# Kernel optimization log

Hardware: AMD Instinct MI355X
Metric: run time of the kernel (lower is better)

The kernel has to match this reference:

```python
import jax, jax.numpy as jnp
import numpy as np

B, C, D, DE, NH = 4, 4, 96, 96, 3
NS, HIN, TOTAL_Z, PZ = 12, 128, 64, 32
WZ = WH = WW = 4
N_WIN_TOK = WZ * WH * WW  # 64 tokens per 3D window


def _rel_index():
    # standard Swin-3D relative position index, (N, N) into a (7*7*7, NH) table
    c = np.stack(np.meshgrid(np.arange(WZ), np.arange(WH), np.arange(WW), indexing='ij')).reshape(3, -1)
    r = (c[:, :, None] - c[:, None, :]).transpose(1, 2, 0)
    r += np.array([WZ - 1, WH - 1, WW - 1])
    r[:, :, 0] *= (2 * WH - 1) * (2 * WW - 1)
    r[:, :, 1] *= (2 * WW - 1)
    return jnp.asarray(r.sum(-1))

REL_IDX = _rel_index()


def layernorm(x, g, b, eps=1e-5):
    m = x.mean(-1, keepdims=True)
    v = x.var(-1, keepdims=True)
    return (x - m) * jax.lax.rsqrt(v + eps) * g + b


def groupnorm(x, g, b, groups=8, eps=1e-5):
    Bb, Cc, Z, H, W = x.shape
    xr = x.reshape(Bb, groups, Cc // groups, Z, H, W)
    m = xr.mean((2, 3, 4, 5), keepdims=True)
    v = xr.var((2, 3, 4, 5), keepdims=True)
    xr = (xr - m) * jax.lax.rsqrt(v + eps)
    return xr.reshape(Bb, Cc, Z, H, W) * g[None, :, None, None, None] + b[None, :, None, None, None]


def conv3d(x, w, b):
    y = jax.lax.conv_general_dilated(x, w, (1, 1, 1), 'SAME', dimension_numbers=('NCDHW', 'OIDHW', 'NCDHW'))
    return y + b[None, :, None, None, None]


def z_interp(x, pos, out_z):
    """Linear interp along z. x:(B,C,S,H,W), pos:(S,) sorted float positions.
    Matches the torch loop: clamp below first / above last, weight=0.5 on ties."""
    S = x.shape[2]
    zq = jnp.arange(out_z, dtype=jnp.float32)
    right = jnp.searchsorted(pos, zq, side='left')  # first i with pos[i] >= z
    left = jnp.clip(right - 1, 0, S - 1)
    rc = jnp.clip(right, 0, S - 1)
    lp, rp = pos[left], pos[rc]
    d = rp - lp
    w = jnp.where(d > 0, (zq - lp) / jnp.where(d > 0, d, 1.0), 0.5)
    w = w[None, None, :, None, None]
    return (1.0 - w) * x[:, :, left] + w * x[:, :, rc]


def reference(sparse_obs, encoder_feat, pe_w, pe_b, pe_g, pe_beta, enc_w, enc_b, ln_g, ln_b,
              qkv_w, qkv_b, attn_w, attn_b, rpb, ref_w1, ref_b1, gn1_g, gn1_b,
              ref_w2, ref_b2, gn2_g, gn2_b, rec_w, rec_b, sparse_indices):
    Bb, Cc, Sz, H, W = sparse_obs.shape
    pos = sparse_indices.astype(jnp.float32)
    # --- skip connection: z-interp baseline at full resolution ---
    baseline = z_interp(sparse_obs, pos, TOTAL_Z)  # (B,C,64,128,128)
    # --- sparse patch embed: conv (1,4,4) stride (1,4,4) + LN ---
    xr = sparse_obs.reshape(Bb, Cc, Sz, H // 4, 4, W // 4, 4)
    f = jnp.einsum('bczhpwq,dcpq->bdzhw', xr, pe_w) + pe_b[None, :, None, None, None]
    f = layernorm(f.transpose(0, 2, 3, 4, 1), pe_g, pe_beta).transpose(0, 4, 1, 2, 3)
    # position-aware z interpolation into patch space (patch_size_z = 2)
    f = z_interp(f, pos / 2.0, PZ)  # (B,D,32,32,32)
    # --- encoder 1x1x1 projection + fuse ---
    enc = jnp.einsum('bczhw,dc->bdzhw', encoder_feat, enc_w) + enc_b[None, :, None, None, None]
    f = f + enc
    # --- 3D window attention with relative position bias (pre-norm, residual) ---
    nz = PZ // WZ
    x = f.transpose(0, 2, 3, 4, 1)  # (B,Z,H,W,D)
    xw = x.reshape(Bb, nz, WZ, nz, WH, nz, WW, D).transpose(0, 1, 3, 5, 2, 4, 6, 7).reshape(-1, N_WIN_TOK, D)
    sc = xw
    xn = layernorm(xw, ln_g, ln_b)
    dh = D // NH
    qkv = (xn @ qkv_w.T + qkv_b).reshape(-1, N_WIN_TOK, 3, NH, dh).transpose(2, 0, 3, 1, 4)
    q, k, v = qkv[0], qkv[1], qkv[2]  # (nWin*B, NH, N, dh)
    att = jnp.einsum('whnd,whmd->whnm', q * (dh ** -0.5), k)
    att = att + rpb[REL_IDX].transpose(2, 0, 1)[None]  # (.., NH, N, N)
    att = jax.nn.softmax(att, axis=-1)
    o = jnp.einsum('whnm,whmd->whnd', att, v).transpose(0, 2, 1, 3).reshape(-1, N_WIN_TOK, D)
    xw = sc + (o @ attn_w.T + attn_b)
    x = xw.reshape(Bb, nz, nz, nz, WZ, WH, WW, D).transpose(0, 1, 4, 2, 5, 3, 6, 7).reshape(Bb, PZ, PZ, PZ, D)
    f = x.transpose(0, 4, 1, 2, 3)
    f = jax.nn.gelu(groupnorm(conv3d(f, ref_w1, ref_b1), gn1_g, gn1_b), approximate=False)
    f = jax.nn.gelu(groupnorm(conv3d(f, ref_w2, ref_b2), gn2_g, gn2_b), approximate=False)
    # --- patch recovery: ConvTranspose3d kernel=stride=(2,4,4) as einsum+reshape ---
    delta = jnp.einsum('bizhw,iodef->bozdhewf', f, rec_w).reshape(Bb, Cc, PZ * 2, PZ * 4, PZ * 4)
    delta = delta + rec_b[None, :, None, None, None]
    return baseline + delta


def setup_inputs():
    key = jax.random.key(0)
    ks = jax.random.split(key, 16)
    n = lambda i, shape: jax.random.normal(ks[i], shape, dtype=jnp.float32) * 0.02
    return {
        'sparse_obs': jax.random.normal(ks[0], (B, C, NS, HIN, HIN), dtype=jnp.float32),
        'encoder_feat': jax.random.normal(ks[1], (B, DE, PZ, PZ, PZ), dtype=jnp.float32),
        'pe_w': n(2, (D, C, 4, 4)), 'pe_b': jnp.zeros((D,)), 'pe_g': jnp.ones((D,)), 'pe_beta': jnp.zeros((D,)),
        'enc_w': n(3, (D, DE)), 'enc_b': jnp.zeros((D,)),
        'ln_g': jnp.ones((D,)), 'ln_b': jnp.zeros((D,)),
        'qkv_w': n(4, (3 * D, D)), 'qkv_b': jnp.zeros((3 * D,)),
        'attn_w': n(5, (D, D)), 'attn_b': jnp.zeros((D,)),
        'rpb': n(6, ((2 * WZ - 1) * (2 * WH - 1) * (2 * WW - 1), NH)),
        'ref_w1': n(7, (D, D, 3, 3, 3)), 'ref_b1': jnp.zeros((D,)), 'gn1_g': jnp.ones((D,)), 'gn1_b': jnp.zeros((D,)),
        'ref_w2': n(8, (D, D, 3, 3, 3)), 'ref_b2': jnp.zeros((D,)), 'gn2_g': jnp.ones((D,)), 'gn2_b': jnp.zeros((D,)),
        'rec_w': n(9, (D, C, 2, 4, 4)), 'rec_b': jnp.zeros((C,)),
        'sparse_indices': jnp.asarray(np.round(np.linspace(0, 63, 12)).astype(np.int64)),
    }
```

## Files before the change

kernel.cpp:

```cpp
#include <hip/hip_runtime.h>
#include <math.h>

typedef __attribute__((ext_vector_type(8))) short short8v;
typedef __attribute__((ext_vector_type(4))) float float4v;

__device__ inline unsigned short f2bf(float f) {
  unsigned u = __float_as_uint(f);
  return (unsigned short)((u + 0x7fff + ((u >> 16) & 1)) >> 16);
}
__device__ inline unsigned pk2(float a, float b) {
  return (unsigned)f2bf(a) | ((unsigned)f2bf(b) << 16);
}
__device__ inline float bfl(unsigned u) { return __uint_as_float(u << 16); }
__device__ inline float bfh(unsigned u) { return __uint_as_float(u & 0xffff0000u); }
__device__ inline float bfs(short s) { return __uint_as_float(((unsigned)(unsigned short)s) << 16); }

__global__ __launch_bounds__(96) void k_tables(const int* __restrict__ sidx, int* __restrict__ T) {
  __shared__ float pos[12];
  int t = threadIdx.x;
  if (t < 12) pos[t] = (float)sidx[t];
  __syncthreads();
  if (t < 64) {
    float zq = (float)t;
    int r = 0;
    while (r < 12 && pos[r] < zq) r++;
    int l = r - 1; if (l < 0) l = 0; if (l > 11) l = 11;
    int rc = r; if (rc > 11) rc = 11;
    float lp = pos[l], rp = pos[rc], d = rp - lp;
    float w = d > 0.f ? (zq - lp) / d : 0.5f;
    T[t] = l; T[64 + t] = rc; ((float*)T)[128 + t] = w;
  } else {
    int zq = t - 64;
    float zqf = (float)zq;
    int r = 0;
    while (r < 12 && pos[r] * 0.5f < zqf) r++;
    int l = r - 1; if (l < 0) l = 0; if (l > 11) l = 11;
    int rc = r; if (rc > 11) rc = 11;
    float lp = pos[l] * 0.5f, rp = pos[rc] * 0.5f, d = rp - lp;
    float w = d > 0.f ? (zqf - lp) / d : 0.5f;
    T[192 + zq] = l; T[224 + zq] = rc; ((float*)T)[256 + zq] = w;
  }
}

__global__ __launch_bounds__(256) void k_wcv(const float* __restrict__ w, short* __restrict__ Wt) {
  int id = blockIdx.x * 256 + threadIdx.x;
  if (id >= 248832) return;
  float v = w[id];
  int o = id / 2592; int rem = id % 2592; int i = rem / 27; int tap = rem % 27;
  Wt[(tap * 96 + o) * 96 + i] = (short)f2bf(v);
}

__global__ __launch_bounds__(256) void k_cvt(const float* __restrict__ src, short* __restrict__ dst, int n) {
  int id = blockIdx.x * 256 + threadIdx.x;
  if (id < n) dst[id] = (short)f2bf(src[id]);
}

__global__ __launch_bounds__(256) void k_wrt(const float* __restrict__ src, short* __restrict__ dst) {
  int id = blockIdx.x * 256 + threadIdx.x;
  if (id >= 12288) return;
  int i = id >> 7, j = id & 127;
  dst[j * 96 + i] = (short)f2bf(src[id]);
}

__global__ __launch_bounds__(256) void k_bias(const float* __restrict__ rpb, float* __restrict__ Bt) {
  int id = blockIdx.x * 256 + threadIdx.x;
  if (id >= 12288) return;
  int head = id >> 12, rem = id & 4095, n = rem >> 6, m = rem & 63;
  int dz = (n >> 4) - (m >> 4), dh = ((n >> 2) & 3) - ((m >> 2) & 3), dw = (n & 3) - (m & 3);
  Bt[id] = rpb[((dz + 3) * 49 + (dh + 3) * 7 + (dw + 3)) * 3 + head];
}

__global__ __launch_bounds__(256) void k_pe(const float* __restrict__ sp, const short* __restrict__ Wpe,
    const float* __restrict__ pb, const float* __restrict__ pg, const float* __restrict__ pbeta,
    float* __restrict__ f1) {
  int x = blockIdx.x;
  int b = x / 384, z = (x / 32) % 12, h = x % 32;
  __shared__ short sB[32][72];
  __shared__ float sF[32][97];
  __shared__ float sM[32], sR[32];
  int tid = threadIdx.x;
  for (int id = tid; id < 2048; id += 256) {
    int c = id >> 9, p = (id >> 7) & 3, col = id & 127;
    float v = sp[(((b * 4 + c) * 12 + z) * 128 + h * 4 + p) * 128 + col];
    sB[col >> 2][c * 16 + p * 4 + (col & 3)] = (short)f2bf(v);
  }
  __syncthreads();
  int w = tid >> 6, l = tid & 63, lo = l & 15, ig = l >> 4;
  int nt = w & 1, mbase = (w >> 1) * 3;
  short8v bfrag[2];
  #pragma unroll
  for (int kc = 0; kc < 2; kc++)
    bfrag[kc] = *(const short8v*)&sB[nt * 16 + lo][kc * 32 + ig * 8];
  #pragma unroll
  for (int mi = 0; mi < 3; mi++) {
    int m = mbase + mi;
    float4v acc = (float4v){0.f, 0.f, 0.f, 0.f};
    #pragma unroll
    for (int kc = 0; kc < 2; kc++) {
      short8v a = *(const short8v*)(Wpe + (size_t)(m * 16 + lo) * 64 + kc * 32 + ig * 8);
      acc = __builtin_amdgcn_mfma_f32_16x16x32_bf16(a, bfrag[kc], acc, 0, 0, 0);
    }
    int wcoord = nt * 16 + lo;
    #pragma unroll
    for (int r = 0; r < 4; r++) {
      int d = m * 16 + ig * 4 + r;
      sF[wcoord][d] = acc[r] + pb[d];
    }
  }
  __syncthreads();
  if (tid < 32) {
    int wv = tid;
    float s = 0.f, ss = 0.f;
    for (int d = 0; d < 96; d++) { float v = sF[wv][d]; s += v; ss += v * v; }
    float m = s * (1.f / 96.f);
    float var = ss * (1.f / 96.f) - m * m;
    sM[wv] = m; sR[wv] = rsqrtf(var + 1e-5f);
  }
  __syncthreads();
  for (int id = tid; id < 3072; id += 256) {
    int d = id >> 5, wv = id & 31;
    float v = (sF[wv][d] - sM[wv]) * sR[wv] * pg[d] + pbeta[d];
    f1[(((b * 96 + d) * 12 + z) * 32 + h) * 32 + wv] = v;
  }
}

__global__ __launch_bounds__(256) void k_ie(const float* __restrict__ f1, const float* __restrict__ ef,
    const short* __restrict__ Wenc, const float* __restrict__ eb, const int* __restrict__ T,
    unsigned* __restrict__ Xg) {
  int x = blockIdx.x;
  int b = x >> 9, chunk = x & 511;
  int v0 = chunk * 64;
  int z = v0 >> 10, rp = v0 & 1023;
  int zl = T[192 + z], zr = T[224 + z];
  float wt = ((const float*)T)[256 + z];
  __shared__ short sEb[64][104];
  int tid = threadIdx.x;
  for (int id = tid; id < 6144; id += 256) {
    int c = id >> 6, vs = id & 63;
    sEb[vs][c] = (short)f2bf(ef[(size_t)(b * 96 + c) * 32768 + v0 + vs]);
  }
  __syncthreads();
  int w = tid >> 6, l = tid & 63, lo = l & 15, ig = l >> 4;
  int vcol = w * 16 + lo;
  short8v bfrag[3];
  #pragma unroll
  for (int kc = 0; kc < 3; kc++)
    bfrag[kc] = *(const short8v*)&sEb[vcol][kc * 32 + ig * 8];
  float4v acc[6];
  #pragma unroll
  for (int m = 0; m < 6; m++) {
    acc[m] = (float4v){0.f, 0.f, 0.f, 0.f};
    #pragma unroll
    for (int kc = 0; kc < 3; kc++) {
      short8v a = *(const short8v*)(Wenc + (size_t)(m * 16 + lo) * 96 + kc * 32 + ig * 8);
      acc[m] = __builtin_amdgcn_mfma_f32_16x16x32_bf16(a, bfrag[kc], acc[m], 0, 0, 0);
    }
  }
  int zb = z >> 2, tz = z & 3;
  int h0 = (chunk & 15) * 2;
  int h = h0 + (vcol >> 5), wc = vcol & 31;
  int win = ((b * 8 + zb) * 8 + (h >> 2)) * 8 + (wc >> 2);
  int t = tz * 16 + (h & 3) * 4 + (wc & 3);
  size_t xbase = (size_t)(win * 64 + t) * 48;
  float wl = 1.f - wt;
  #pragma unroll
  for (int m = 0; m < 6; m++) {
    #pragma unroll
    for (int rr = 0; rr < 2; rr++) {
      int d0 = m * 16 + ig * 4 + rr * 2;
      const float* p1a = f1 + ((size_t)(b * 96 + d0) * 12 + zl) * 1024 + rp + vcol;
      const float* p2a = f1 + ((size_t)(b * 96 + d0) * 12 + zr) * 1024 + rp + vcol;
      const float* p1b = f1 + ((size_t)(b * 96 + d0 + 1) * 12 + zl) * 1024 + rp + vcol;
      const float* p2b = f1 + ((size_t)(b * 96 + d0 + 1) * 12 + zr) * 1024 + rp + vcol;
      float va = acc[m][rr * 2] + eb[d0] + wl * p1a[0] + wt * p2a[0];
      float vb = acc[m][rr * 2 + 1] + eb[d0 + 1] + wl * p1b[0] + wt * p2b[0];
      Xg[xbase + m * 8 + ig * 2 + rr] = pk2(va, vb);
    }
  }
}

__global__ __launch_bounds__(256) void k_fatt(const unsigned* __restrict__ Xg,
    const short* __restrict__ Wq, const float* __restrict__ qb,
    const float* __restrict__ lg, const float* __restrict__ lb,
    const short* __restrict__ Wa, const float* __restrict__ ab,
    const float* __restrict__ Bt, short* __restrict__ Xt) {
  int win = blockIdx.x;
  __shared__ short sA[64][104];
  __shared__ short sN[64][104];
  __shared__ short sK[192][40];
  __shared__ short sVt[96][88];
  __shared__ short sQP[4][16][104];
  __shared__ float sMn[64], sRs[64];
  int tid = threadIdx.x;
  int w = tid >> 6, l = tid & 63, lo = l & 15, ig = l >> 4;
  const float scale = 0.17677669529663687f;

  for (int id = tid; id < 3072; id += 256) {
    int row = id / 48, c2 = id % 48;
    *(unsigned*)&sA[row][c2 * 2] = Xg[(size_t)(win * 64 + row) * 48 + c2];
  }
  __syncthreads();
  {
    int token = tid >> 2, jl = tid & 3;
    float s = 0.f, ss = 0.f;
    #pragma unroll
    for (int i = 0; i < 12; i++) {
      unsigned u = *(unsigned*)&sA[token][jl * 24 + i * 2];
      float v0 = bfl(u), v1 = bfh(u);
      s += v0 + v1; ss += v0 * v0 + v1 * v1;
    }
    s += __shfl_xor(s, 1); ss += __shfl_xor(ss, 1);
    s += __shfl_xor(s, 2); ss += __shfl_xor(ss, 2);
    if (jl == 0) {
      float m = s * (1.f / 96.f);
      sMn[token] = m;
      sRs[token] = rsqrtf(ss * (1.f / 96.f) - m * m + 1e-5f);
    }
  }
  __syncthreads();
  for (int id = tid; id < 3072; id += 256) {
    int row = id / 48, c2 = id % 48;
    unsigned u = *(unsigned*)&sA[row][c2 * 2];
    float m = sMn[row], r = sRs[row];
    float v0 = (bfl(u) - m) * r * lg[2 * c2] + lb[2 * c2];
    float v1 = (bfh(u) - m) * r * lg[2 * c2 + 1] + lb[2 * c2 + 1];
    *(unsigned*)&sN[row][c2 * 2] = pk2(v0, v1);
  }
  __syncthreads();
  {
    short8v a[3];
    #pragma unroll
    for (int kc = 0; kc < 3; kc++)
      a[kc] = *(const short8v*)&sN[w * 16 + lo][kc * 32 + ig * 8];
    for (int nt = 0; nt < 18; nt++) {
      float4v acc = (float4v){0.f, 0.f, 0.f, 0.f};
      #pragma unroll
      for (int kc = 0; kc < 3; kc++) {
        short8v bfr = *(const short8v*)(Wq + (size_t)(nt * 16 + lo) * 96 + kc * 32 + ig * 8);
        acc = __builtin_amdgcn_mfma_f32_16x16x32_bf16(a[kc], bfr, acc, 0, 0, 0);
      }
      int out = nt * 16 + lo;
      float bias = qb[out];
      if (nt < 6) {
        int head = out >> 5, c = out & 31;
        #pragma unroll
        for (int r = 0; r < 4; r++)
          sQP[w][ig * 4 + r][head * 32 + c] = (short)f2bf((acc[r] + bias) * scale);
      } else if (nt < 12) {
        int o2 = out - 96, head = o2 >> 5, c = o2 & 31;
        #pragma unroll
        for (int r = 0; r < 4; r++)
          sK[head * 64 + w * 16 + ig * 4 + r][c] = (short)f2bf(acc[r] + bias);
      } else {
        int o2 = out - 192;
        #pragma unroll
        for (int r = 0; r < 4; r++)
          sVt[o2][w * 16 + ig * 4 + r] = (short)f2bf(acc[r] + bias);
      }
    }
  }
  __syncthreads();
  short8v qf[3];
  #pragma unroll
  for (int h = 0; h < 3; h++)
    qf[h] = *(const short8v*)&sQP[w][lo][h * 32 + ig * 8];
  for (int h = 0; h < 3; h++) {
    short8v kf[4];
    #pragma unroll
    for (int nt = 0; nt < 4; nt++)
      kf[nt] = *(const short8v*)&sK[h * 64 + nt * 16 + lo][ig * 8];
    float4v s[4];
    #pragma unroll
    for (int nt = 0; nt < 4; nt++)
      s[nt] = __builtin_amdgcn_mfma_f32_16x16x32_bf16(qf[h], kf[nt], (float4v){0.f, 0.f, 0.f, 0.f}, 0, 0, 0);
    const float* bt = Bt + h * 4096;
    #pragma unroll
    for (int r = 0; r < 4; r++) {
      int tok = w * 16 + ig * 4 + r;
      float v[4];
      float mx = -1e30f;
      #pragma unroll
      for (int nt = 0; nt < 4; nt++) {
        v[nt] = s[nt][r] + bt[tok * 64 + nt * 16 + lo];
        mx = fmaxf(mx, v[nt]);
      }
      mx = fmaxf(mx, __shfl_xor(mx, 1));
      mx = fmaxf(mx, __shfl_xor(mx, 2));
      mx = fmaxf(mx, __shfl_xor(mx, 4));
      mx = fmaxf(mx, __shfl_xor(mx, 8));
      float sm = 0.f;
      #pragma unroll
      for (int nt = 0; nt < 4; nt++) { v[nt] = __expf(v[nt] - mx); sm += v[nt]; }
      sm += __shfl_xor(sm, 1);
      sm += __shfl_xor(sm, 2);
      sm += __shfl_xor(sm, 4);
      sm += __shfl_xor(sm, 8);
      float inv = 1.f / sm;
      #pragma unroll
      for (int nt = 0; nt < 4; nt++)
        sQP[w][ig * 4 + r][nt * 16 + lo] = (short)f2bf(v[nt] * inv);
    }
    short8v pa[2];
    #pragma unroll
    for (int kc = 0; kc < 2; kc++)
      pa[kc] = *(const short8v*)&sQP[w][lo][kc * 32 + ig * 8];
    #pragma unroll
    for (int ct = 0; ct < 2; ct++) {
      short8v vb0 = *(const short8v*)&sVt[h * 32 + ct * 16 + lo][ig * 8];
      short8v vb1 = *(const short8v*)&sVt[h * 32 + ct * 16 + lo][32 + ig * 8];
      float4v o = __builtin_amdgcn_mfma_f32_16x16x32_bf16(pa[0], vb0, (float4v){0.f, 0.f, 0.f, 0.f}, 0, 0, 0);
      o = __builtin_amdgcn_mfma_f32_16x16x32_bf16(pa[1], vb1, o, 0, 0, 0);
      #pragma unroll
      for (int r = 0; r < 4; r++)
        sA[w * 16 + ig * 4 + r][h * 32 + ct * 16 + lo] = (short)f2bf(o[r]);
    }
  }
  {
    short8v a[3];
    #pragma unroll
    for (int kc = 0; kc < 3; kc++)
      a[kc] = *(const short8v*)&sA[w * 16 + lo][kc * 32 + ig * 8];
    #pragma unroll
    for (int nt = 0; nt < 6; nt++) {
      float4v acc = (float4v){0.f, 0.f, 0.f, 0.f};
      #pragma unroll
      for (int kc = 0; kc < 3; kc++) {
        short8v bfr = *(const short8v*)(Wa + (size_t)(nt * 16 + lo) * 96 + kc * 32 + ig * 8);
        acc = __builtin_amdgcn_mfma_f32_16x16x32_bf16(a[kc], bfr, acc, 0, 0, 0);
      }
      int out = nt * 16 + lo;
      float bias = ab[out];
      #pragma unroll
      for (int r = 0; r < 4; r++) {
        int tok = w * 16 + ig * 4 + r;
        unsigned u = Xg[(size_t)(win * 64 + tok) * 48 + (out >> 1)];
        float res = (out & 1) ? bfh(u) : bfl(u);
        sN[tok][out] = (short)f2bf(acc[r] + bias + res);
      }
    }
  }
  __syncthreads();
  int b = win >> 9, zb = (win >> 6) & 7, hb = (win >> 3) & 7, wb = win & 7;
  for (int id = tid; id < 3072; id += 256) {
    int cc = id >> 10, rem = id & 1023, t = rem >> 4, ilp = rem & 15;
    unsigned pk = *(unsigned*)&sN[t][cc * 32 + ilp * 2];
    int tz = t >> 4, th = (t >> 2) & 3, tw = t & 3;
    size_t vox = (size_t)(zb * 4 + tz) * 1024 + (hb * 4 + th) * 32 + wb * 4 + tw;
    ((unsigned*)Xt)[((size_t)(b * 3 + cc) * 32768 + vox) * 16 + ilp] = pk;
  }
}

__global__ __launch_bounds__(256) void k_convM(const short* __restrict__ Xt,
    const short* __restrict__ Wt, const float* __restrict__ cb, short* __restrict__ y16,
    float* __restrict__ stats) {
  int x = blockIdx.x;
  int b = x >> 7, zp = (x >> 3) & 15, hq = x & 7;
  int tid = threadIdx.x;
  int wvi = tid >> 6, l = tid & 63;
  int lo = l & 15, ig = l >> 4;
  int hp = wvi & 1, mh = wvi >> 1;
  __shared__ short Xl[816 * 32];
  __shared__ float sG[16];
  if (tid < 16) sG[tid] = 0.f;
  float4v acc[3][2][2][2];
  #pragma unroll
  for (int mi = 0; mi < 3; mi++)
    #pragma unroll
    for (int zo = 0; zo < 2; zo++)
      #pragma unroll
      for (int hr = 0; hr < 2; hr++)
        #pragma unroll
        for (int n = 0; n < 2; n++) acc[mi][zo][hr][n] = (float4v){0.f, 0.f, 0.f, 0.f};

  for (int c = 0; c < 3; c++) {
    __syncthreads();
    for (int r = 0; r < 13; r++) {
      int id = tid + 256 * r;
      if (id < 3264) {
        int seg = id & 3, q = id >> 2;
        int zz = q / 204, rem = q - zz * 204;
        int hh = rem / 34, ww = rem - hh * 34;
        int gz = zp * 2 + zz - 1, gh = hq * 4 + hh - 1, gw = ww - 1;
        int4 val = {0, 0, 0, 0};
        if (gz >= 0 && gz < 32 && gh >= 0 && gh < 32 && gw >= 0 && gw < 32)
          val = *(const int4*)(Xt + ((size_t)((b * 3 + c) * 32768 + (gz << 10) + (gh << 5) + gw) * 32 + seg * 8));
        int slot = seg ^ ((q >> 1) & 3);
        *(int4*)(&Xl[q * 32 + slot * 8]) = val;
      }
    }
    __syncthreads();
    for (int dh = 0; dh < 3; dh++) {
      for (int dwv = 0; dwv < 3; dwv++) {
        short8v bfr[4][2][2];
        #pragma unroll
        for (int zr = 0; zr < 4; zr++)
          #pragma unroll
          for (int hr = 0; hr < 2; hr++)
            #pragma unroll
            for (int n = 0; n < 2; n++) {
              int vox = (zr * 6 + hp * 2 + hr + dh) * 34 + n * 16 + lo + dwv;
              bfr[zr][hr][n] = *(const short8v*)&Xl[vox * 32 + ((ig ^ ((vox >> 1) & 3)) * 8)];
            }
        #pragma unroll
        for (int dz = 0; dz < 3; dz++) {
          int tap = dz * 9 + dh * 3 + dwv;
          #pragma unroll
          for (int mi = 0; mi < 3; mi++) {
            short8v wf = *(const short8v*)(Wt +
                ((size_t)(tap * 96 + (mh * 3 + mi) * 16 + lo)) * 96 + c * 32 + ig * 8);
            #pragma unroll
            for (int zo = 0; zo < 2; zo++)
              #pragma unroll
              for (int hr = 0; hr < 2; hr++)
                #pragma unroll
                for (int n = 0; n < 2; n++)
                  acc[mi][zo][hr][n] = __builtin_amdgcn_mfma_f32_16x16x32_bf16(wf, bfr[zo + dz][hr][n], acc[mi][zo][hr][n], 0, 0, 0);
          }
        }
      }
    }
  }
  #pragma unroll
  for (int mi = 0; mi < 3; mi++) {
    #pragma unroll
    for (int r = 0; r < 4; r++) {
      int o = (mh * 3 + mi) * 16 + ig * 4 + r;
      float cbo = cb[o];
      float s = 0.f, ss = 0.f;
      #pragma unroll
      for (int zo = 0; zo < 2; zo++)
        #pragma unroll
        for (int hr = 0; hr < 2; hr++)
          #pragma unroll
          for (int n = 0; n < 2; n++) {
            float v = acc[mi][zo][hr][n][r] + cbo;
            int z = zp * 2 + zo;
            int h = hq * 4 + hp * 2 + hr;
            int vcol = n * 16 + lo;
            y16[((size_t)(b * 96 + o) << 15) + (z << 10) + (h << 5) + vcol] = (short)f2bf(v);
            s += v; ss += v * v;
          }
      s += __shfl_xor(s, 1); ss += __shfl_xor(ss, 1);
      s += __shfl_xor(s, 2); ss += __shfl_xor(ss, 2);
      s += __shfl_xor(s, 4); ss += __shfl_xor(ss, 4);
      s += __shfl_xor(s, 8); ss += __shfl_xor(ss, 8);
      if (lo == 0) {
        int gl = o / 12;
        atomicAdd(&sG[gl * 2], s);
        atomicAdd(&sG[gl * 2 + 1], ss);
      }
    }
  }
  __syncthreads();
  if (tid < 16) atomicAdd(&stats[b * 16 + tid], sG[tid]);
}

__global__ __launch_bounds__(256) void k_gn(const short* __restrict__ y16, const float* __restrict__ stats,
    const float* __restrict__ gg, const float* __restrict__ gb, short* __restrict__ xt) {
  int x = blockIdx.x;
  int b = x / 1536, r = x % 1536, c = r / 512, vt = r % 512;
  int v0 = vt * 64;
  __shared__ float sT[64][33];
  int tid = threadIdx.x;
  const float invN = 1.f / 393216.f;
  {
    int ol = tid >> 3, vq = tid & 7;
    int o = c * 32 + ol, g = b * 8 + o / 12;
    float m = stats[2 * g] * invN;
    float var = stats[2 * g + 1] * invN - m * m;
    float rs = rsqrtf(var + 1e-5f) * gg[o];
    float bb = gb[o];
    short8v yv = *(const short8v*)&y16[((size_t)(b * 96 + o) << 15) + v0 + vq * 8];
    #pragma unroll
    for (int j = 0; j < 8; j++) {
      float val = (bfs(yv[j]) - m) * rs + bb;
      sT[vq * 8 + j][ol] = 0.5f * val * (1.f + erff(val * 0.70710678118654752f));
    }
  }
  __syncthreads();
  for (int id = tid; id < 1024; id += 256) {
    int v = id >> 4, p = id & 15;
    ((unsigned*)xt)[((size_t)(b * 3 + c) * 32768 + v0 + v) * 16 + p] = pk2(sT[v][2 * p], sT[v][2 * p + 1]);
  }
}

__global__ __launch_bounds__(256) void k_final(const short* __restrict__ f5b, const float* __restrict__ sp,
    const short* __restrict__ Wrec, const float* __restrict__ rb, const int* __restrict__ T,
    float* __restrict__ out) {
  int x = blockIdx.x;
  int b = x >> 10, chunk = x & 1023;
  int z = chunk >> 5, h = chunk & 31;
  int v0 = chunk * 32;
  int tid = threadIdx.x;
  int w = tid >> 6, l = tid & 63, lo = l & 15, ig = l >> 4;
  short8v afrag[2][3];
  #pragma unroll
  for (int mt = 0; mt < 2; mt++)
    #pragma unroll
    for (int kc = 0; kc < 3; kc++)
      afrag[mt][kc] = *(const short8v*)(f5b +
          ((size_t)(b * 3 + kc) * 32768 + v0 + mt * 16 + lo) * 32 + ig * 8);
  float4v acc[2][2];
  #pragma unroll
  for (int nt2 = 0; nt2 < 2; nt2++) {
    int jt = w * 2 + nt2;
    #pragma unroll
    for (int mt = 0; mt < 2; mt++) acc[mt][nt2] = (float4v){0.f, 0.f, 0.f, 0.f};
    #pragma unroll
    for (int kc = 0; kc < 3; kc++) {
      short8v bfr = *(const short8v*)(Wrec + (size_t)(jt * 16 + lo) * 96 + kc * 32 + ig * 8);
      #pragma unroll
      for (int mt = 0; mt < 2; mt++)
        acc[mt][nt2] = __builtin_amdgcn_mfma_f32_16x16x32_bf16(afrag[mt][kc], bfr, acc[mt][nt2], 0, 0, 0);
    }
  }
  const float* w64 = (const float*)(T + 128);
  #pragma unroll
  for (int mt = 0; mt < 2; mt++)
    #pragma unroll
    for (int nt2 = 0; nt2 < 2; nt2++) {
      int jt = w * 2 + nt2;
      #pragma unroll
      for (int r = 0; r < 4; r++) {
        int wv = mt * 16 + ig * 4 + r;
        int j = jt * 16 + lo;
        int o = j >> 5, dd = (j >> 4) & 1, e = (j >> 2) & 3, ff = j & 3;
        int Z = 2 * z + dd, H = 4 * h + e, W = 4 * wv + ff;
        int zl = T[Z], zr = T[64 + Z];
        float bw = w64[Z];
        const float* spb = sp + (size_t)(b * 4 + o) * 196608;
        float bval = (1.f - bw) * spb[(size_t)zl * 16384 + H * 128 + W]
                   + bw * spb[(size_t)zr * 16384 + H * 128 + W];
        out[((size_t)(b * 4 + o) * 64 + Z) * 16384 + H * 128 + W] = bval + acc[mt][nt2][r] + rb[o];
      }
    }
}

extern "C" void kernel_launch(void* const* d_in, const int* in_sizes, int n_in,
                              void* d_out, int out_size, void* d_ws, size_t ws_size,
                              hipStream_t stream) {
  const float* sp    = (const float*)d_in[0];
  const float* ef    = (const float*)d_in[1];
  const float* pe_w  = (const float*)d_in[2];
  const float* pe_b  = (const float*)d_in[3];
  const float* pe_g  = (const float*)d_in[4];
  const float* pe_be = (const float*)d_in[5];
  const float* enc_w = (const float*)d_in[6];
  const float* enc_b = (const float*)d_in[7];
  const float* ln_g  = (const float*)d_in[8];
  const float* ln_b  = (const float*)d_in[9];
  const float* qkv_w = (const float*)d_in[10];
  const float* qkv_b = (const float*)d_in[11];
  const float* at_w  = (const float*)d_in[12];
  const float* at_b  = (const float*)d_in[13];
  const float* rpb   = (const float*)d_in[14];
  const float* w1    = (const float*)d_in[15];
  const float* b1    = (const float*)d_in[16];
  const float* g1g   = (const float*)d_in[17];
  const float* g1b   = (const float*)d_in[18];
  const float* w2    = (const float*)d_in[19];
  const float* b2    = (const float*)d_in[20];
  const float* g2g   = (const float*)d_in[21];
  const float* g2b   = (const float*)d_in[22];
  const float* recw  = (const float*)d_in[23];
  const float* recb  = (const float*)d_in[24];
  const int*   sidx  = (const int*)d_in[25];
  float* out = (float*)d_out;

  char* ws = (char*)d_ws;
  unsigned* Xg = (unsigned*)ws;
  float* f1    = (float*)(ws + 25165824);
  short* XtA   = (short*)(ws + 25165824);
  short* Y16   = (short*)(ws + 50331648);
  int*   T     = (int*)(ws + 100663296);
  float* stats = (float*)(ws + 100665344);
  short* Wrec  = (short*)(ws + 100666368);

  char* dob = (char*)d_out;
  short* Wenc = (short*)(dob + 25165824);
  short* Wpe  = (short*)(dob + 25184256);
  short* Wqkv = (short*)(dob + 65937408);
  short* Waw  = (short*)(dob + 65992704);
  float* Bt   = (float*)(dob + 66011136);
  short* Wt1  = (short*)(dob + 66060288);
  short* Wt2  = (short*)(dob + 66557952);

  k_tables<<<1, 96, 0, stream>>>(sidx, T);
  k_wcv<<<972, 256, 0, stream>>>(w1, Wt1);
  k_wcv<<<972, 256, 0, stream>>>(w2, Wt2);
  k_cvt<<<108, 256, 0, stream>>>(qkv_w, Wqkv, 27648);
  k_cvt<<<36, 256, 0, stream>>>(at_w, Waw, 9216);
  k_cvt<<<36, 256, 0, stream>>>(enc_w, Wenc, 9216);
  k_cvt<<<24, 256, 0, stream>>>(pe_w, Wpe, 6144);
  k_wrt<<<48, 256, 0, stream>>>(recw, Wrec);
  k_bias<<<48, 256, 0, stream>>>(rpb, Bt);

  k_pe<<<1536, 256, 0, stream>>>(sp, Wpe, pe_b, pe_g, pe_be, f1);
  k_ie<<<2048, 256, 0, stream>>>(f1, ef, Wenc, enc_b, T, Xg);
  k_fatt<<<2048, 256, 0, stream>>>(Xg, Wqkv, qkv_b, ln_g, ln_b, Waw, at_b, Bt, XtA);

  hipMemsetAsync(stats, 0, 64 * sizeof(float), stream);
  k_convM<<<512, 256, 0, stream>>>(XtA, Wt1, b1, Y16, stats);
  k_gn<<<6144, 256, 0, stream>>>(Y16, stats, g1g, g1b, XtA);

  hipMemsetAsync(stats, 0, 64 * sizeof(float), stream);
  k_convM<<<512, 256, 0, stream>>>(XtA, Wt2, b2, Y16, stats);
  k_gn<<<6144, 256, 0, stream>>>(Y16, stats, g2g, g2b, XtA);

  k_final<<<4096, 256, 0, stream>>>(XtA, sp, Wrec, recb, T, out);
}
```

Measured before the change: 359.9 us.

## Merge prep kernels, fold layernorm into QKV load, split conv work across more blocks

Nine small weight-conversion and table kernels become a single k_prep launch to cut launch overhead. In the attention kernel the separate layernorm pass and its sN buffer are removed: normalization is applied while loading the MFMA A fragments. The K buffer is unpadded and uses an XOR swizzle, which shrinks LDS. The 3D conv now splits output channels into halves across twice as many blocks, with each wave handling one z slice, so it needs fewer accumulators. This may raise occupancy, at the cost of loading each input halo tile twice.

```diff
diff --git a/kernel.cpp b/kernel.cpp
--- a/kernel.cpp
+++ b/kernel.cpp
@@ -15,59 +15,80 @@
 __device__ inline float bfh(unsigned u) { return __uint_as_float(u & 0xffff0000u); }
 __device__ inline float bfs(short s) { return __uint_as_float(((unsigned)(unsigned short)s) << 16); }
 
-__global__ __launch_bounds__(96) void k_tables(const int* __restrict__ sidx, int* __restrict__ T) {
-  __shared__ float pos[12];
-  int t = threadIdx.x;
-  if (t < 12) pos[t] = (float)sidx[t];
-  __syncthreads();
-  if (t < 64) {
-    float zq = (float)t;
-    int r = 0;
-    while (r < 12 && pos[r] < zq) r++;
-    int l = r - 1; if (l < 0) l = 0; if (l > 11) l = 11;
-    int rc = r; if (rc > 11) rc = 11;
-    float lp = pos[l], rp = pos[rc], d = rp - lp;
-    float w = d > 0.f ? (zq - lp) / d : 0.5f;
-    T[t] = l; T[64 + t] = rc; ((float*)T)[128 + t] = w;
+__global__ __launch_bounds__(256) void k_prep(
+    const int* __restrict__ sidx, int* __restrict__ T,
+    const float* __restrict__ w1, short* __restrict__ Wt1,
+    const float* __restrict__ w2, short* __restrict__ Wt2,
+    const float* __restrict__ qkvw, short* __restrict__ Wqkv,
+    const float* __restrict__ atw, short* __restrict__ Waw,
+    const float* __restrict__ encw, short* __restrict__ Wenc,
+    const float* __restrict__ pew, short* __restrict__ Wpe,
+    const float* __restrict__ recw, short* __restrict__ Wrec,
+    const float* __restrict__ rpb, float* __restrict__ Bt) {
+  int bx = blockIdx.x;
+  int tid = threadIdx.x;
+  if (bx < 1944) {
+    const float* w = bx < 972 ? w1 : w2;
+    short* Wt = bx < 972 ? Wt1 : Wt2;
+    int id = (bx < 972 ? bx : bx - 972) * 256 + tid;
+    if (id < 248832) {
+      float v = w[id];
+      int o = id / 2592; int rem = id % 2592; int i = rem / 27; int tap = rem % 27;
+      Wt[(tap * 96 + o) * 96 + i] = (short)f2bf(v);
+    }
+  } else if (bx < 2052) {
+    int id = (bx - 1944) * 256 + tid;
+    if (id < 27648) Wqkv[id] = (short)f2bf(qkvw[id]);
+  } else if (bx < 2088) {
+    int id = (bx - 2052) * 256 + tid;
+    if (id < 9216) Waw[id] = (short)f2bf(atw[id]);
+  } else if (bx < 2124) {
+    int id = (bx - 2088) * 256 + tid;
+    if (id < 9216) Wenc[id] = (short)f2bf(encw[id]);
+  } else if (bx < 2148) {
+    int id = (bx - 2124) * 256 + tid;
+    if (id < 6144) Wpe[id] = (short)f2bf(pew[id]);
+  } else if (bx < 2196) {
+    int id = (bx - 2148) * 256 + tid;
+    if (id < 12288) {
+      int i = id >> 7, j = id & 127;
+      Wrec[j * 96 + i] = (short)f2bf(recw[id]);
+    }
+  } else if (bx < 2244) {
+    int id = (bx - 2196) * 256 + tid;
+    if (id < 12288) {
+      int head = id >> 12, rem = id & 4095, n = rem >> 6, m = rem & 63;
+      int dz = (n >> 4) - (m >> 4), dh = ((n >> 2) & 3) - ((m >> 2) & 3), dw = (n & 3) - (m & 3);
+      Bt[id] = rpb[((dz + 3) * 49 + (dh + 3) * 7 + (dw + 3)) * 3 + head];
+    }
   } else {
-    int zq = t - 64;
-    float zqf = (float)zq;
-    int r = 0;
-    while (r < 12 && pos[r] * 0.5f < zqf) r++;
-    int l = r - 1; if (l < 0) l = 0; if (l > 11) l = 11;
-    int rc = r; if (rc > 11) rc = 11;
-    float lp = pos[l] * 0.5f, rp = pos[rc] * 0.5f, d = rp - lp;
-    float w = d > 0.f ? (zqf - lp) / d : 0.5f;
-    T[192 + zq] = l; T[224 + zq] = rc; ((float*)T)[256 + zq] = w;
-  }
-}
-
-__global__ __launch_bounds__(256) void k_wcv(const float* __restrict__ w, short* __restrict__ Wt) {
-  int id = blockIdx.x * 256 + threadIdx.x;
-  if (id >= 248832) return;
-  float v = w[id];
-  int o = id / 2592; int rem = id % 2592; int i = rem / 27; int tap = rem % 27;
-  Wt[(tap * 96 + o) * 96 + i] = (short)f2bf(v);
-}
-
-__global__ __launch_bounds__(256) void k_cvt(const float* __restrict__ src, short* __restrict__ dst, int n) {
-  int id = blockIdx.x * 256 + threadIdx.x;
-  if (id < n) dst[id] = (short)f2bf(src[id]);
-}
-
-__global__ __launch_bounds__(256) void k_wrt(const float* __restrict__ src, short* __restrict__ dst) {
-  int id = blockIdx.x * 256 + threadIdx.x;
-  if (id >= 12288) return;
-  int i = id >> 7, j = id & 127;
-  dst[j * 96 + i] = (short)f2bf(src[id]);
-}
-
-__global__ __launch_bounds__(256) void k_bias(const float* __restrict__ rpb, float* __restrict__ Bt) {
-  int id = blockIdx.x * 256 + threadIdx.x;
-  if (id >= 12288) return;
-  int head = id >> 12, rem = id & 4095, n = rem >> 6, m = rem & 63;
-  int dz = (n >> 4) - (m >> 4), dh = ((n >> 2) & 3) - ((m >> 2) & 3), dw = (n & 3) - (m & 3);
-  Bt[id] = rpb[((dz + 3) * 49 + (dh + 3) * 7 + (dw + 3)) * 3 + head];
+    __shared__ float pos[12];
+    int t = tid;
+    if (t < 12) pos[t] = (float)sidx[t];
+    __syncthreads();
+    if (t < 64) {
+      float zq = (float)t;
+      int r = 0;
+      while (r < 12 && pos[r] < zq) r++;
+      int lft = r - 1; if (lft < 0) lft = 0; if (lft > 11) lft = 11;
+      int rc = r; if (rc > 11) rc = 11;
+      float lp = pos[lft], rp = pos[rc], d = rp - lp;
+      float w = d > 0.f ? (zq - lp) / d : 0.5f;
+      T[t] = lft; T[64 + t] = rc; ((float*)T)[128 + t] = w;
+    } else if (t < 128) {
+      int zq = t - 64;
+      float zqf = (float)zq;
+      if (zq < 32) {
+        int r = 0;
+        while (r < 12 && pos[r] * 0.5f < zqf) r++;
+        int lft = r - 1; if (lft < 0) lft = 0; if (lft > 11) lft = 11;
+        int rc = r; if (rc > 11) rc = 11;
+        float lp = pos[lft] * 0.5f, rp = pos[rc] * 0.5f, d = rp - lp;
+        float w = d > 0.f ? (zqf - lp) / d : 0.5f;
+        T[192 + zq] = lft; T[224 + zq] = rc; ((float*)T)[256 + zq] = w;
+      }
+    }
+  }
 }
 
 __global__ __launch_bounds__(256) void k_pe(const float* __restrict__ sp, const short* __restrict__ Wpe,
@@ -186,10 +207,9 @@
     const float* __restrict__ Bt, short* __restrict__ Xt) {
   int win = blockIdx.x;
   __shared__ short sA[64][104];
-  __shared__ short sN[64][104];
-  __shared__ short sK[192][40];
-  __shared__ short sVt[96][88];
-  __shared__ short sQP[4][16][104];
+  __shared__ short sQP[4][16][96];
+  __shared__ short sK[192][32];
+  __shared__ short sVt[96][72];
   __shared__ float sMn[64], sRs[64];
   int tid = threadIdx.x;
   int w = tid >> 6, l = tid & 63, lo = l & 15, ig = l >> 4;
@@ -218,20 +238,22 @@
     }
   }
   __syncthreads();
-  for (int id = tid; id < 3072; id += 256) {
-    int row = id / 48, c2 = id % 48;
-    unsigned u = *(unsigned*)&sA[row][c2 * 2];
-    float m = sMn[row], r = sRs[row];
-    float v0 = (bfl(u) - m) * r * lg[2 * c2] + lb[2 * c2];
-    float v1 = (bfh(u) - m) * r * lg[2 * c2 + 1] + lb[2 * c2 + 1];
-    *(unsigned*)&sN[row][c2 * 2] = pk2(v0, v1);
-  }
-  __syncthreads();
   {
+    int tok = w * 16 + lo;
+    float m = sMn[tok], rr = sRs[tok];
     short8v a[3];
     #pragma unroll
-    for (int kc = 0; kc < 3; kc++)
-      a[kc] = *(const short8v*)&sN[w * 16 + lo][kc * 32 + ig * 8];
+    for (int kc = 0; kc < 3; kc++) {
+      short8v raw = *(const short8v*)&sA[tok][kc * 32 + ig * 8];
+      short8v t;
+      #pragma unroll
+      for (int jj = 0; jj < 8; jj++) {
+        int c = kc * 32 + ig * 8 + jj;
+        float v = (bfs(raw[jj]) - m) * rr * lg[c] + lb[c];
+        t[jj] = (short)f2bf(v);
+      }
+      a[kc] = t;
+    }
     for (int nt = 0; nt < 18; nt++) {
       float4v acc = (float4v){0.f, 0.f, 0.f, 0.f};
       #pragma unroll
@@ -249,8 +271,11 @@
       } else if (nt < 12) {
         int o2 = out - 96, head = o2 >> 5, c = o2 & 31;
         #pragma unroll
-        for (int r = 0; r < 4; r++)
-          sK[head * 64 + w * 16 + ig * 4 + r][c] = (short)f2bf(acc[r] + bias);
+        for (int r = 0; r < 4; r++) {
+          int row = head * 64 + w * 16 + ig * 4 + r;
+          ((short*)sK)[row * 32 + (((c >> 3) ^ ((row >> 1) & 3)) << 3) + (c & 7)] =
+              (short)f2bf(acc[r] + bias);
+        }
       } else {
         int o2 = out - 192;
         #pragma unroll
@@ -267,8 +292,10 @@
   for (int h = 0; h < 3; h++) {
     short8v kf[4];
     #pragma unroll
-    for (int nt = 0; nt < 4; nt++)
-      kf[nt] = *(const short8v*)&sK[h * 64 + nt * 16 + lo][ig * 8];
+    for (int nt = 0; nt < 4; nt++) {
+      int row = h * 64 + nt * 16 + lo;
+      kf[nt] = *(const short8v*)&((short*)sK)[row * 32 + ((ig ^ ((row >> 1) & 3)) << 3)];
+    }
     float4v s[4];
     #pragma unroll
     for (int nt = 0; nt < 4; nt++)
@@ -335,7 +362,7 @@
         int tok = w * 16 + ig * 4 + r;
         unsigned u = Xg[(size_t)(win * 64 + tok) * 48 + (out >> 1)];
         float res = (out & 1) ? bfh(u) : bfl(u);
-        sN[tok][out] = (short)f2bf(acc[r] + bias + res);
+        sA[tok][out] = (short)f2bf(acc[r] + bias + res);
       }
     }
   }
@@ -343,7 +370,7 @@
   int b = win >> 9, zb = (win >> 6) & 7, hb = (win >> 3) & 7, wb = win & 7;
   for (int id = tid; id < 3072; id += 256) {
     int cc = id >> 10, rem = id & 1023, t = rem >> 4, ilp = rem & 15;
-    unsigned pk = *(unsigned*)&sN[t][cc * 32 + ilp * 2];
+    unsigned pk = *(unsigned*)&sA[t][cc * 32 + ilp * 2];
     int tz = t >> 4, th = (t >> 2) & 3, tw = t & 3;
     size_t vox = (size_t)(zb * 4 + tz) * 1024 + (hb * 4 + th) * 32 + wb * 4 + tw;
     ((unsigned*)Xt)[((size_t)(b * 3 + cc) * 32768 + vox) * 16 + ilp] = pk;
@@ -354,23 +381,21 @@
     const short* __restrict__ Wt, const float* __restrict__ cb, short* __restrict__ y16,
     float* __restrict__ stats) {
   int x = blockIdx.x;
-  int b = x >> 7, zp = (x >> 3) & 15, hq = x & 7;
+  int oh = x & 1, hq = (x >> 1) & 7, zp = (x >> 4) & 15, b = x >> 8;
   int tid = threadIdx.x;
   int wvi = tid >> 6, l = tid & 63;
   int lo = l & 15, ig = l >> 4;
-  int hp = wvi & 1, mh = wvi >> 1;
+  int hp = wvi & 1, zo = wvi >> 1;
   __shared__ short Xl[816 * 32];
   __shared__ float sG[16];
   if (tid < 16) sG[tid] = 0.f;
-  float4v acc[3][2][2][2];
+  float4v acc[3][2][2];
   #pragma unroll
   for (int mi = 0; mi < 3; mi++)
     #pragma unroll
-    for (int zo = 0; zo < 2; zo++)
-      #pragma unroll
-      for (int hr = 0; hr < 2; hr++)
-        #pragma unroll
-        for (int n = 0; n < 2; n++) acc[mi][zo][hr][n] = (float4v){0.f, 0.f, 0.f, 0.f};
+    for (int hr = 0; hr < 2; hr++)
+      #pragma unroll
+      for (int n = 0; n < 2; n++) acc[mi][hr][n] = (float4v){0.f, 0.f, 0.f, 0.f};
 
   for (int c = 0; c < 3; c++) {
     __syncthreads();
@@ -391,15 +416,15 @@
     __syncthreads();
     for (int dh = 0; dh < 3; dh++) {
       for (int dwv = 0; dwv < 3; dwv++) {
-        short8v bfr[4][2][2];
+        short8v bfr[3][2][2];
         #pragma unroll
-        for (int zr = 0; zr < 4; zr++)
+        for (int dzr = 0; dzr < 3; dzr++)
           #pragma unroll
           for (int hr = 0; hr < 2; hr++)
             #pragma unroll
             for (int n = 0; n < 2; n++) {
-              int vox = (zr * 6 + hp * 2 + hr + dh) * 34 + n * 16 + lo + dwv;
-              bfr[zr][hr][n] = *(const short8v*)&Xl[vox * 32 + ((ig ^ ((vox >> 1) & 3)) * 8)];
+              int vox = ((zo + dzr) * 6 + hp * 2 + hr + dh) * 34 + n * 16 + lo + dwv;
+              bfr[dzr][hr][n] = *(const short8v*)&Xl[vox * 32 + ((ig ^ ((vox >> 1) & 3)) * 8)];
             }
         #pragma unroll
         for (int dz = 0; dz < 3; dz++) {
@@ -407,39 +432,35 @@
           #pragma unroll
           for (int mi = 0; mi < 3; mi++) {
             short8v wf = *(const short8v*)(Wt +
-                ((size_t)(tap * 96 + (mh * 3 + mi) * 16 + lo)) * 96 + c * 32 + ig * 8);
+                ((size_t)(tap * 96 + oh * 48 + mi * 16 + lo)) * 96 + c * 32 + ig * 8);
             #pragma unroll
-            for (int zo = 0; zo < 2; zo++)
+            for (int hr = 0; hr < 2; hr++)
               #pragma unroll
-              for (int hr = 0; hr < 2; hr++)
-                #pragma unroll
-                for (int n = 0; n < 2; n++)
-                  acc[mi][zo][hr][n] = __builtin_amdgcn_mfma_f32_16x16x32_bf16(wf, bfr[zo + dz][hr][n], acc[mi][zo][hr][n], 0, 0, 0);
+              for (int n = 0; n < 2; n++)
+                acc[mi][hr][n] = __builtin_amdgcn_mfma_f32_16x16x32_bf16(wf, bfr[dz][hr][n], acc[mi][hr][n], 0, 0, 0);
           }
         }
       }
     }
   }
+  int z = zp * 2 + zo;
   #pragma unroll
   for (int mi = 0; mi < 3; mi++) {
     #pragma unroll
     for (int r = 0; r < 4; r++) {
-      int o = (mh * 3 + mi) * 16 + ig * 4 + r;
+      int o = oh * 48 + mi * 16 + ig * 4 + r;
       float cbo = cb[o];
       float s = 0.f, ss = 0.f;
       #pragma unroll
-      for (int zo = 0; zo < 2; zo++)
+      for (int hr = 0; hr < 2; hr++)
         #pragma unroll
-        for (int hr = 0; hr < 2; hr++)
-          #pragma unroll
-          for (int n = 0; n < 2; n++) {
-            float v = acc[mi][zo][hr][n][r] + cbo;
-            int z = zp * 2 + zo;
-            int h = hq * 4 + hp * 2 + hr;
-            int vcol = n * 16 + lo;
-            y16[((size_t)(b * 96 + o) << 15) + (z << 10) + (h << 5) + vcol] = (short)f2bf(v);
-            s += v; ss += v * v;
-          }
+        for (int n = 0; n < 2; n++) {
+          float v = acc[mi][hr][n][r] + cbo;
+          int h = hq * 4 + hp * 2 + hr;
+          int vcol = n * 16 + lo;
+          y16[((size_t)(b * 96 + o) << 15) + (z << 10) + (h << 5) + vcol] = (short)f2bf(v);
+          s += v; ss += v * v;
+        }
       s += __shfl_xor(s, 1); ss += __shfl_xor(ss, 1);
       s += __shfl_xor(s, 2); ss += __shfl_xor(ss, 2);
       s += __shfl_xor(s, 4); ss += __shfl_xor(ss, 4);
@@ -585,26 +606,19 @@
   short* Wt1  = (short*)(dob + 66060288);
   short* Wt2  = (short*)(dob + 66557952);
 
-  k_tables<<<1, 96, 0, stream>>>(sidx, T);
-  k_wcv<<<972, 256, 0, stream>>>(w1, Wt1);
-  k_wcv<<<972, 256, 0, stream>>>(w2, Wt2);
-  k_cvt<<<108, 256, 0, stream>>>(qkv_w, Wqkv, 27648);
-  k_cvt<<<36, 256, 0, stream>>>(at_w, Waw, 9216);
-  k_cvt<<<36, 256, 0, stream>>>(enc_w, Wenc, 9216);
-  k_cvt<<<24, 256, 0, stream>>>(pe_w, Wpe, 6144);
-  k_wrt<<<48, 256, 0, stream>>>(recw, Wrec);
-  k_bias<<<48, 256, 0, stream>>>(rpb, Bt);
+  k_prep<<<2245, 256, 0, stream>>>(sidx, T, w1, Wt1, w2, Wt2, qkv_w, Wqkv,
+                                   at_w, Waw, enc_w, Wenc, pe_w, Wpe, recw, Wrec, rpb, Bt);
 
   k_pe<<<1536, 256, 0, stream>>>(sp, Wpe, pe_b, pe_g, pe_be, f1);
   k_ie<<<2048, 256, 0, stream>>>(f1, ef, Wenc, enc_b, T, Xg);
   k_fatt<<<2048, 256, 0, stream>>>(Xg, Wqkv, qkv_b, ln_g, ln_b, Waw, at_b, Bt, XtA);
 
   hipMemsetAsync(stats, 0, 64 * sizeof(float), stream);
-  k_convM<<<512, 256, 0, stream>>>(XtA, Wt1, b1, Y16, stats);
+  k_convM<<<1024, 256, 0, stream>>>(XtA, Wt1, b1, Y16, stats);
   k_gn<<<6144, 256, 0, stream>>>(Y16, stats, g1g, g1b, XtA);
 
   hipMemsetAsync(stats, 0, 64 * sizeof(float), stream);
-  k_convM<<<512, 256, 0, stream>>>(XtA, Wt2, b2, Y16, stats);
+  k_convM<<<1024, 256, 0, stream>>>(XtA, Wt2, b2, Y16, stats);
   k_gn<<<6144, 256, 0, stream>>>(Y16, stats, g2g, g2b, XtA);
 
   k_final<<<4096, 256, 0, stream>>>(XtA, sp, Wrec, recb, T, out);
```

After: 399.3 us. 11.0% more time.
